# Performance work log

Measured on AMD Instinct MI355X. Metric: run time of the kernel, lower is better.

## Reference

```python
import jax, jax.numpy as jnp
import numpy as np

T_STEPS, BATCH, DX, DH = 128, 128, 1024, 1024
N_GATES = 5


def setup_inputs() -> dict:
    key = jax.random.key(0)
    ks = jax.random.split(key, 4)
    scale_x = 1.0 / np.sqrt(DX)
    scale_h = 1.0 / np.sqrt(DH)
    inputs = jax.random.normal(ks[0], (T_STEPS, BATCH, DX), dtype=jnp.float32)
    memories = jax.random.normal(ks[1], (T_STEPS, BATCH, DH), dtype=jnp.float32)
    h0 = jnp.zeros((BATCH, DH), dtype=jnp.float32)
    c0 = jnp.zeros((BATCH, DH), dtype=jnp.float32)
    Wx = jax.random.normal(ks[2], (N_GATES * DH, DX), dtype=jnp.float32) * scale_x
    bx = jnp.zeros((N_GATES * DH,), dtype=jnp.float32)
    Wh = jax.random.normal(ks[3], (N_GATES * DH, DH), dtype=jnp.float32) * scale_h
    # forget-gate bias (second chunk) initialized to 1, as in reset_parameters_
    bh = jnp.zeros((N_GATES * DH,), dtype=jnp.float32).at[DH:2 * DH].set(1.0)
    return {"inputs": inputs, "memories": memories, "h0": h0, "c0": c0,
            "Wx": Wx, "bx": bx, "Wh": Wh, "bh": bh}


def reference(inputs, memories, h0, c0, Wx, bx, Wh, bh):
    # EpLSTMCell.loop: time-major scan of the custom gated cell.
    # Gate order: I, F, G, O, R (tied forget gate: it = 1 - ft).
    def step(carry, inp):
        h, c = carry
        xt, mt = inp
        gx = jnp.dot(xt, Wx.T) + bx      # [B, 5*Dh]
        gh = jnp.dot(h, Wh.T) + bh       # [B, 5*Dh]
        Xi, Xf, Xg, Xo, Xr = jnp.split(gx, N_GATES, axis=-1)
        Hi, Hf, Hg, Ho, Hr = jnp.split(gh, N_GATES, axis=-1)
        ft = jax.nn.sigmoid(Xf + Hf)
        ot = jax.nn.sigmoid(Xo + Ho)
        it = 1.0 - ft                    # tied forget gate
        gt = jnp.tanh(Xg + Hg)
        rt = jax.nn.sigmoid(Xr + Hr)     # episodic memory gate
        ct = ft * c + it * gt + rt * jnp.tanh(mt)
        ht = ot * jnp.tanh(ct)
        return (ht, ct), ht

    (_, _), outs = jax.lax.scan(step, (h0, c0), (inputs, memories))
    return outs  # [T, B, Dh]
```

## Files before the change

### kernel.cpp

```cpp
#include <hip/hip_runtime.h>

#define T_STEPS 128
#define BATCH   128
#define DX      1024
#define DH      1024
#define BDH     (BATCH * DH)
#define BDX     (BATCH * DX)
#define PLW     40

typedef __attribute__((ext_vector_type(8)))  short short8;
typedef __attribute__((ext_vector_type(16))) float f32x16;
typedef __attribute__((ext_vector_type(4)))  float f32x4v;
typedef __attribute__((ext_vector_type(2)))  float f32x2;
typedef __attribute__((ext_vector_type(4)))  unsigned u32x4;

static __device__ __forceinline__ unsigned short f2bf(float f) {
    union { float f; unsigned u; } v; v.f = f;
    unsigned r = v.u + 0x7fffu + ((v.u >> 16) & 1u);
    return (unsigned short)(r >> 16);
}
static __device__ __forceinline__ short8 pack_bf16x8(f32x4v lo, f32x4v hi) {
    union { unsigned short u[8]; short8 v; } pk;
    pk.u[0]=f2bf(lo[0]); pk.u[1]=f2bf(lo[1]); pk.u[2]=f2bf(lo[2]); pk.u[3]=f2bf(lo[3]);
    pk.u[4]=f2bf(hi[0]); pk.u[5]=f2bf(hi[1]); pk.u[6]=f2bf(hi[2]); pk.u[7]=f2bf(hi[3]);
    return pk.v;
}
static __device__ __forceinline__ float sigf(float x) {
    float u = __expf(-fabsf(x));
    float b = 1.0f / (1.0f + u);
    return x >= 0.0f ? b : 1.0f - b;
}
static __device__ __forceinline__ float tanhfast(float x) {
    float u = __expf(-2.0f * fabsf(x));
    float r = (1.0f - u) / (1.0f + u);
    return x >= 0.0f ? r : -r;
}


__global__ __launch_bounds__(256) void prep_x(const float* __restrict__ x,
                                              unsigned short* __restrict__ Xb) {
    const size_t i8 = ((size_t)blockIdx.x * 256 + threadIdx.x) * 8;
    f32x4v lo = __builtin_nontemporal_load((const f32x4v*)(x + i8));
    f32x4v hi = __builtin_nontemporal_load((const f32x4v*)(x + i8 + 4));
    short8 v = pack_bf16x8(lo, hi);
    __builtin_nontemporal_store(v, (short8*)(Xb + i8));
}

__global__ __launch_bounds__(256) void init_seed(const float* __restrict__ h0,
                                                 unsigned short* __restrict__ hseq,
                                                 unsigned* __restrict__ gflag) {
    const int i = blockIdx.x * 256 + threadIdx.x;
    if (i < BDH) hseq[i] = f2bf(h0[i]);
    if (blockIdx.x < 2) gflag[blockIdx.x * 256 + threadIdx.x] = 0;
}

__global__ __launch_bounds__(128) void prep_wxp(const float* __restrict__ Wx,
                                                const float* __restrict__ bx,
                                                const float* __restrict__ bh,
                                                unsigned short* __restrict__ Wxp,
                                                float* __restrict__ bp) {
    const int p = blockIdx.x;
    const int js = p >> 5, g = (p >> 3) & 3, jj = p & 7;
    const int srow = (g + 1) * 1024 + js * 8 + jj;
    const int k = threadIdx.x * 8;
    f32x4v lo = __builtin_nontemporal_load((const f32x4v*)(Wx + (size_t)srow * DX + k));
    f32x4v hi = __builtin_nontemporal_load((const f32x4v*)(Wx + (size_t)srow * DX + k + 4));
    short8 v = pack_bf16x8(lo, hi);
    __builtin_nontemporal_store(v, (short8*)(Wxp + (size_t)p * 1024 + k));
    if (threadIdx.x == 0) bp[p] = bx[srow] + bh[srow];
}

template<bool XBF16>
__global__ __launch_bounds__(256, 1) void gx_prepass2(
    const void* __restrict__ xsrc, const unsigned short* __restrict__ Wxp,
    const float* __restrict__ bp, _Float16* __restrict__ Gx)
{
    extern __shared__ char sm[];
    _Float16* pl16 = (_Float16*)(sm + 131072);

    const int bid = blockIdx.x;
    const int c  = bid & 7;
    const int jp = bid >> 3;
    const int tid = threadIdx.x;

    {
        const int row = tid >> 2;
        const int chunk = tid & 3;
        const int sw = (row & 7) << 4;
        const unsigned short* src = Wxp + (size_t)(jp * 64 + row) * 1024;
        char* dst = sm + row * 2048;
        #pragma unroll
        for (int j = 0; j < 32; ++j) {
            const int off = chunk * 16 + j * 64;
            short8 v = __builtin_nontemporal_load((const short8*)(src + (off >> 1)));
            *(short8*)(dst + (off ^ sw)) = v;
        }
    }

    const int rrow = tid >> 1;
    const int jjb  = (tid & 1) * 4;
    float bias_f[2][16];
    #pragma unroll
    for (int jsl = 0; jsl < 2; ++jsl)
        #pragma unroll
        for (int q = 0; q < 4; ++q)
            #pragma unroll
            for (int g = 0; g < 4; ++g)
                bias_f[jsl][q * 4 + g] = bp[(jp * 2 + jsl) * 32 + g * 8 + (jjb + q)];

    const int wave = tid >> 6, lane = tid & 63;
    const int k8 = (lane >> 5) * 8;
    const char* wrow0 = sm + (lane & 31) * 2048;
    const char* wrow1 = wrow0 + 32 * 2048;
    const int sw2 = ((lane & 31) & 7) << 4;
    __syncthreads();

    for (int i = 0; i < 16; ++i) {
        const int mt = c * 16 + i;
        const int arow = mt * 128 + wave * 32 + (lane & 31);
        f32x16 a00 = {}, a01 = {}, a10 = {}, a11 = {};

        if (XBF16) {
            const unsigned short* xp = (const unsigned short*)xsrc + (size_t)arow * 1024 + k8;
            #pragma unroll 8
            for (int ks = 0; ks < 64; ++ks) {
                short8 a  = *(const short8*)(xp + ks * 16);
                short8 b0 = *(const short8*)(wrow0 + ((ks * 32 + k8 * 2) ^ sw2));
                short8 b1 = *(const short8*)(wrow1 + ((ks * 32 + k8 * 2) ^ sw2));
                if (ks & 1) {
                    a01 = __builtin_amdgcn_mfma_f32_32x32x16_bf16(a, b0, a01, 0, 0, 0);
                    a11 = __builtin_amdgcn_mfma_f32_32x32x16_bf16(a, b1, a11, 0, 0, 0);
                } else {
                    a00 = __builtin_amdgcn_mfma_f32_32x32x16_bf16(a, b0, a00, 0, 0, 0);
                    a10 = __builtin_amdgcn_mfma_f32_32x32x16_bf16(a, b1, a10, 0, 0, 0);
                }
            }
        } else {
            const float* Af = (const float*)xsrc + (size_t)arow * 1024 + k8;
            #pragma unroll 8
            for (int ks = 0; ks < 64; ++ks) {
                f32x4v lo = *(const f32x4v*)(Af + ks * 16);
                f32x4v hi = *(const f32x4v*)(Af + ks * 16 + 4);
                union { unsigned u32[4]; short8 v; } pk;
                pk.u32[0] = __builtin_amdgcn_perm(__float_as_uint(lo[1]), __float_as_uint(lo[0]), 0x07060302u);
                pk.u32[1] = __builtin_amdgcn_perm(__float_as_uint(lo[3]), __float_as_uint(lo[2]), 0x07060302u);
                pk.u32[2] = __builtin_amdgcn_perm(__float_as_uint(hi[1]), __float_as_uint(hi[0]), 0x07060302u);
                pk.u32[3] = __builtin_amdgcn_perm(__float_as_uint(hi[3]), __float_as_uint(hi[2]), 0x07060302u);
                short8 b0 = *(const short8*)(wrow0 + ((ks * 32 + k8 * 2) ^ sw2));
                short8 b1 = *(const short8*)(wrow1 + ((ks * 32 + k8 * 2) ^ sw2));
                if (ks & 1) {
                    a01 = __builtin_amdgcn_mfma_f32_32x32x16_bf16(pk.v, b0, a01, 0, 0, 0);
                    a11 = __builtin_amdgcn_mfma_f32_32x32x16_bf16(pk.v, b1, a11, 0, 0, 0);
                } else {
                    a00 = __builtin_amdgcn_mfma_f32_32x32x16_bf16(pk.v, b0, a00, 0, 0, 0);
                    a10 = __builtin_amdgcn_mfma_f32_32x32x16_bf16(pk.v, b1, a10, 0, 0, 0);
                }
            }
        }
        f32x16 r0 = a00 + a01;
        f32x16 r1 = a10 + a11;

        #pragma unroll
        for (int ii = 0; ii < 16; ++ii) {
            const int rowc = (ii & 3) + 8 * (ii >> 2) + 4 * (lane >> 5);
            pl16[(wave * 32 + rowc) * 72 + (lane & 31)]      = (_Float16)r0[ii];
            pl16[(wave * 32 + rowc) * 72 + 32 + (lane & 31)] = (_Float16)r1[ii];
        }
        __syncthreads();

        #pragma unroll
        for (int jsl = 0; jsl < 2; ++jsl) {
            union { _Float16 h[16]; u32x4 q[2]; } V;
            #pragma unroll
            for (int q = 0; q < 4; ++q)
                #pragma unroll
                for (int g = 0; g < 4; ++g)
                    V.h[q * 4 + g] = (_Float16)(
                        (float)pl16[rrow * 72 + jsl * 32 + g * 8 + (jjb + q)]
                        + bias_f[jsl][q * 4 + g]);
            _Float16* dst = Gx + ((size_t)(mt * 128 + rrow) * 4096
                                  + (jp * 2 + jsl) * 32 + jjb * 4);
            __builtin_nontemporal_store(V.q[0], (u32x4*)dst);
            __builtin_nontemporal_store(V.q[1], (u32x4*)(dst + 8));
        }
        __syncthreads();
    }
}

__global__ __launch_bounds__(256, 1) void eplstm_h(
    const _Float16* __restrict__ Gx,  const float* __restrict__ mem,
    const float* __restrict__ Wh,     const float* __restrict__ c0,
    unsigned short* __restrict__ hseq, float* __restrict__ out,
    unsigned* __restrict__ gflag)
{
    extern __shared__ char smem[];
    float* pl = (float*)(smem + 65536);

    const int bid = blockIdx.x;
    const int js = bid >> 1, bhh = bid & 1;
    const int tid = threadIdx.x;

    {
        const int row = tid >> 3;
        const int g = row >> 3, jj = row & 7;
        const int srow = (g + 1) * 1024 + js * 8 + jj;
        const int sw = (row & 7) << 4;
        const float* W = Wh + (size_t)srow * 1024;
        char* dst = smem + row * 2048;
        #pragma unroll
        for (int it = 0; it < 16; ++it) {
            const int k = (tid & 7) * 128 + it * 8;
            f32x4v lo = __builtin_nontemporal_load((const f32x4v*)(W + k));
            f32x4v hi = __builtin_nontemporal_load((const f32x4v*)(W + k + 4));
            short8 v = pack_bf16x8(lo, hi);
            *(short8*)(dst + ((k * 2) ^ sw)) = v;
        }
    }

    const int e0 = tid * 2;
    const int row_e = e0 >> 3;
    const int jj0 = e0 & 7;
    const int brow = bhh * 64 + row_e;
    const size_t obase = (size_t)brow * DH + js * 8 + jj0;
    const int mh_e = row_e >> 5, r_e = row_e & 31;
    float2 creg = *(const float2*)(c0 + obase);

    const int wave = tid >> 6, lane = tid & 63;
    const int mh = wave >> 1, kh = wave & 1;
    const int arow = bhh * 64 + mh * 32 + (lane & 31);
    const int k8 = (lane >> 5) * 8;
    const char* wrow = smem + (lane & 31) * 2048;
    const int sw2 = ((lane & 31) & 7) << 4;
    const int kbyte0 = (kh * 512 + k8) * 2;
    const int p = lane & 31;
    const int word = (p & 7) * 4 + (p >> 3);
    float* plw = pl + wave * 32 * PLW;
    unsigned long long* fb = (unsigned long long*)(gflag + bhh * 128);

    __syncthreads();

    for (int t = 0; t < T_STEPS; ++t) {
        u32x4 gxv = __builtin_nontemporal_load(
            (const u32x4*)(Gx + ((size_t)(t * BATCH + brow) * 4096 + js * 32 + jj0 * 4)));
        f32x2 mv = __builtin_nontemporal_load(
            (const f32x2*)(mem + (size_t)t * BDH + obase));

        if (t > 0) {
            if (wave == 0) {
                for (;;) {
                    unsigned long long fv = __hip_atomic_load(
                        &fb[lane], __ATOMIC_RELAXED, __HIP_MEMORY_SCOPE_AGENT);
                    if (__all(((unsigned)fv >= (unsigned)t) &&
                              ((unsigned)(fv >> 32) >= (unsigned)t))) break;
                    __builtin_amdgcn_s_sleep(4);
                }
            }
            __syncthreads();
        }

        const unsigned short* hp = hseq + (size_t)t * BDH + (size_t)arow * DH + kh * 512 + k8;
        f32x16 a0 = {}, a1 = {};
        #pragma unroll 16
        for (int ks = 0; ks < 32; ++ks) {
            short8 a = *(const short8*)(hp + ks * 16);
            short8 b = *(const short8*)(wrow + ((kbyte0 + ks * 32) ^ sw2));
            if (ks & 1) a1 = __builtin_amdgcn_mfma_f32_32x32x16_bf16(a, b, a1, 0, 0, 0);
            else        a0 = __builtin_amdgcn_mfma_f32_32x32x16_bf16(a, b, a0, 0, 0, 0);
        }
        f32x16 r = a0 + a1;
        #pragma unroll
        for (int ii = 0; ii < 16; ++ii) {
            const int rowc = (ii & 3) + 8 * (ii >> 2) + 4 * (lane >> 5);
            plw[rowc * PLW + word] = r[ii];
        }
        __syncthreads();

        float4 p0A = *(const float4*)(pl + (((mh_e << 1) | 0) * 32 + r_e) * PLW + (jj0 + 0) * 4);
        float4 p0B = *(const float4*)(pl + (((mh_e << 1) | 1) * 32 + r_e) * PLW + (jj0 + 0) * 4);
        float4 p1A = *(const float4*)(pl + (((mh_e << 1) | 0) * 32 + r_e) * PLW + (jj0 + 1) * 4);
        float4 p1B = *(const float4*)(pl + (((mh_e << 1) | 1) * 32 + r_e) * PLW + (jj0 + 1) * 4);
        union { u32x4 u; _Float16 h[8]; } G; G.u = gxv;

        float hv[2];
        {
            const float gF = (float)G.h[0] + p0A.x + p0B.x;
            const float gG = (float)G.h[1] + p0A.y + p0B.y;
            const float gO = (float)G.h[2] + p0A.z + p0B.z;
            const float gR = (float)G.h[3] + p0A.w + p0B.w;
            const float ft = sigf(gF), ot = sigf(gO), rt = sigf(gR);
            const float gt = tanhfast(gG);
            const float cv = ft * creg.x + (1.f - ft) * gt + rt * tanhfast(mv[0]);
            creg.x = cv;
            hv[0] = ot * tanhfast(cv);
        }
        {
            const float gF = (float)G.h[4] + p1A.x + p1B.x;
            const float gG = (float)G.h[5] + p1A.y + p1B.y;
            const float gO = (float)G.h[6] + p1A.z + p1B.z;
            const float gR = (float)G.h[7] + p1A.w + p1B.w;
            const float ft = sigf(gF), ot = sigf(gO), rt = sigf(gR);
            const float gt = tanhfast(gG);
            const float cv = ft * creg.y + (1.f - ft) * gt + rt * tanhfast(mv[1]);
            creg.y = cv;
            hv[1] = ot * tanhfast(cv);
        }
        const unsigned hp2 = (unsigned)f2bf(hv[0]) | ((unsigned)f2bf(hv[1]) << 16);
        __hip_atomic_store((unsigned*)(hseq + (size_t)(t + 1) * BDH + obase), hp2,
                           __ATOMIC_RELAXED, __HIP_MEMORY_SCOPE_AGENT);
        f32x2 hvv = { hv[0], hv[1] };
        __builtin_nontemporal_store(hvv, (f32x2*)(out + (size_t)t * BDH + obase));

        asm volatile("s_waitcnt vmcnt(0)" ::: "memory");
        __syncthreads();
        if (tid == 0 && t < T_STEPS - 1) {
            __hip_atomic_store(&gflag[bhh * 128 + js], (unsigned)(t + 1),
                               __ATOMIC_RELAXED, __HIP_MEMORY_SCOPE_AGENT);
        }
    }
}

template<bool XBF16>
__global__ __launch_bounds__(256, 1) void eplstm_persistent(
    const void*  __restrict__ xsrc, const float* __restrict__ mem,
    const float* __restrict__ Wx,   const float* __restrict__ Wh,
    const float* __restrict__ bxp,  const float* __restrict__ bhp,
    const float* __restrict__ c0,
    unsigned short* __restrict__ hseq, float* __restrict__ out,
    unsigned* __restrict__ bar)
{
    extern __shared__ char smem[];
    float* pl = reinterpret_cast<float*>(smem + 131072);

    const int bid = blockIdx.x;
    const int js  = bid >> 1;
    const int bhh = bid & 1;
    const int tid = threadIdx.x;

    {
        const int prow = tid >> 3;
        const int g = prow >> 3, jj = prow & 7;
        const int srow = (g + 1) * 1024 + js * 8 + jj;
        const int kc = (tid & 7) * 256;
        const int sw = (prow & 7) << 4;
        for (int it = 0; it < 32; ++it) {
            const int k = kc + it * 8;
            const float* src = (k < DX) ? (Wx + (size_t)srow * DX + k)
                                        : (Wh + (size_t)srow * DH + (k - DX));
            f32x4v lo = *(const f32x4v*)(src);
            f32x4v hi = *(const f32x4v*)(src + 4);
            short8 v = pack_bf16x8(lo, hi);
            *reinterpret_cast<short8*>(smem + prow * 4096 + ((k * 2) ^ sw)) = v;
        }
    }

    const int e0   = tid * 2;
    const int bl   = e0 >> 3;
    const int jj0  = e0 & 7;
    const int brow_g = bhh * 64 + bl;
    const size_t oidx = (size_t)brow_g * DH + js * 8 + jj0;
    float biasv[2][4];
    #pragma unroll
    for (int e2 = 0; e2 < 2; ++e2)
        #pragma unroll
        for (int g = 0; g < 4; ++g) {
            const int srow = (g + 1) * 1024 + js * 8 + jj0 + e2;
            biasv[e2][g] = bxp[srow] + bhp[srow];
        }
    float2 creg = *reinterpret_cast<const float2*>(c0 + oidx);
    const int mh_e = bl >> 5, rr = bl & 31;

    const int wave = tid >> 6;
    const int lane = tid & 63;
    const int mh = wave >> 1, kh = wave & 1;
    const int arow   = bhh * 64 + mh * 32 + (lane & 31);
    const int k8     = (lane >> 5) * 8;
    const int brow   = lane & 31;
    const char* bbase = smem + brow * 4096;
    const int swz    = (brow & 7) << 4;
    const int kbyte0 = kh * 2048 + k8 * 2;

    __syncthreads();

    for (int t = 0; t < T_STEPS; ++t) {
        f32x16 ac0 = {}, ac1 = {}, ac2 = {}, ac3 = {};
        if (XBF16 || kh == 1) {
            const unsigned short* Ab = kh
                ? (hseq + (size_t)t * BDH + (size_t)arow * DH + k8)
                : ((const unsigned short*)xsrc + (size_t)t * BDX + (size_t)arow * DX + k8);
            #pragma unroll 8
            for (int ks = 0; ks < 64; ++ks) {
                short8 a = *reinterpret_cast<const short8*>(Ab + ks * 16);
                short8 b = *reinterpret_cast<const short8*>(bbase + ((kbyte0 + ks * 32) ^ swz));
                if      ((ks & 3) == 0) ac0 = __builtin_amdgcn_mfma_f32_32x32x16_bf16(a, b, ac0, 0, 0, 0);
                else if ((ks & 3) == 1) ac1 = __builtin_amdgcn_mfma_f32_32x32x16_bf16(a, b, ac1, 0, 0, 0);
                else if ((ks & 3) == 2) ac2 = __builtin_amdgcn_mfma_f32_32x32x16_bf16(a, b, ac2, 0, 0, 0);
                else                    ac3 = __builtin_amdgcn_mfma_f32_32x32x16_bf16(a, b, ac3, 0, 0, 0);
            }
        } else {
            const float* Af = (const float*)xsrc + (size_t)t * BDX + (size_t)arow * DX + k8;
            #pragma unroll 4
            for (int ks = 0; ks < 64; ++ks) {
                f32x4v lo = *(const f32x4v*)(Af + ks * 16);
                f32x4v hi = *(const f32x4v*)(Af + ks * 16 + 4);
                short8 a = pack_bf16x8(lo, hi);
                short8 b = *reinterpret_cast<const short8*>(bbase + ((kbyte0 + ks * 32) ^ swz));
                if      ((ks & 3) == 0) ac0 = __builtin_amdgcn_mfma_f32_32x32x16_bf16(a, b, ac0, 0, 0, 0);
                else if ((ks & 3) == 1) ac1 = __builtin_amdgcn_mfma_f32_32x32x16_bf16(a, b, ac1, 0, 0, 0);
                else if ((ks & 3) == 2) ac2 = __builtin_amdgcn_mfma_f32_32x32x16_bf16(a, b, ac2, 0, 0, 0);
                else                    ac3 = __builtin_amdgcn_mfma_f32_32x32x16_bf16(a, b, ac3, 0, 0, 0);
            }
        }
        f32x16 r = (ac0 + ac1) + (ac2 + ac3);

        #pragma unroll
        for (int i = 0; i < 16; ++i) {
            const int row = (i & 3) + 8 * (i >> 2) + 4 * (lane >> 5);
            pl[(wave * 32 + row) * 33 + brow] = r[i];
        }
        __syncthreads();

        const float2 mt2 = *reinterpret_cast<const float2*>(mem + (size_t)t * BDH + oidx);
        float hv[2];
        #pragma unroll
        for (int e2 = 0; e2 < 2; ++e2) {
            const int jj = jj0 + e2;
            float gs[4];
            #pragma unroll
            for (int g = 0; g < 4; ++g) {
                const int col = g * 8 + jj;
                gs[g] = pl[((mh_e * 2 + 0) * 32 + rr) * 33 + col]
                      + pl[((mh_e * 2 + 1) * 32 + rr) * 33 + col]
                      + biasv[e2][g];
            }
            const float ft = 1.f / (1.f + expf(-gs[0]));
            const float gt = tanhf(gs[1]);
            const float ot = 1.f / (1.f + expf(-gs[2]));
            const float rt = 1.f / (1.f + expf(-gs[3]));
            const float cin = e2 ? creg.y : creg.x;
            const float mv  = e2 ? mt2.y : mt2.x;
            const float cv = ft * cin + (1.f - ft) * gt + rt * tanhf(mv);
            if (e2) creg.y = cv; else creg.x = cv;
            hv[e2] = ot * tanhf(cv);
        }
        *reinterpret_cast<float2*>(out + (size_t)t * BDH + oidx) = make_float2(hv[0], hv[1]);
        const unsigned hp = (unsigned)f2bf(hv[0]) | ((unsigned)f2bf(hv[1]) << 16);
        __hip_atomic_store((unsigned*)(hseq + (size_t)(t + 1) * BDH + oidx), hp,
                           __ATOMIC_RELAXED, __HIP_MEMORY_SCOPE_AGENT);

        __syncthreads();
        if (t < T_STEPS - 1) {
            if (tid == 0) {
                const unsigned want = (unsigned)(t + 1);
                const unsigned arrived = __hip_atomic_fetch_add(
                    &bar[bhh * 32], 1u, __ATOMIC_RELAXED, __HIP_MEMORY_SCOPE_AGENT);
                if (arrived == want * 128u - 1u) {
                    __hip_atomic_store(&bar[64 + bhh * 32], want,
                                       __ATOMIC_RELAXED, __HIP_MEMORY_SCOPE_AGENT);
                } else {
                    while (__hip_atomic_load(&bar[64 + bhh * 32],
                                             __ATOMIC_RELAXED, __HIP_MEMORY_SCOPE_AGENT) < want)
                        __builtin_amdgcn_s_sleep(2);
                }
            }
            __syncthreads();
        }
    }
}

extern "C" void kernel_launch(void* const* d_in, const int* in_sizes, int n_in,
                              void* d_out, int out_size, void* d_ws, size_t ws_size,
                              hipStream_t stream) {
    const float* inputs   = (const float*)d_in[0];
    const float* memories = (const float*)d_in[1];
    const float* h0       = (const float*)d_in[2];
    const float* c0       = (const float*)d_in[3];
    const float* Wx       = (const float*)d_in[4];
    const float* bx       = (const float*)d_in[5];
    const float* Wh       = (const float*)d_in[6];
    const float* bh_      = (const float*)d_in[7];
    float* outp = (float*)d_out;

    char* ws = (char*)d_ws;
    size_t off = 0;
    auto alloc = [&](size_t bytes) {
        char* p = ws + off;
        off = (off + bytes + 255) & ~(size_t)255;
        return p;
    };
    unsigned*       gflag = (unsigned*)alloc(512 * sizeof(unsigned));
    unsigned short* hseq  = (unsigned short*)alloc((size_t)(T_STEPS + 1) * BDH * 2);

    const size_t wxp_b  = (size_t)4096 * 1024 * 2;
    const size_t bp_b   = 4096 * 4;
    const size_t gx_b   = (size_t)16384 * 4096 * 2;
    const size_t xb_b   = (size_t)T_STEPS * BDX * 2;
    const size_t need_base = off + wxp_b + 256 + bp_b + 256 + gx_b + 256;
    const size_t need_xb   = need_base + xb_b + 256;

    if (ws_size >= need_base) {
        unsigned short* Wxp = (unsigned short*)alloc(wxp_b);
        float*          bp  = (float*)alloc(bp_b);
        _Float16*       Gx  = (_Float16*)alloc(gx_b);
        const bool use_xb = (ws_size >= need_xb);
        unsigned short* Xb = use_xb ? (unsigned short*)alloc(xb_b) : nullptr;

        init_seed<<<512, 256, 0, stream>>>(h0, hseq, gflag);
        prep_wxp<<<4096, 128, 0, stream>>>(Wx, bx, bh_, Wxp, bp);

        const unsigned pre_smem = 131072 + 128 * 72 * 2;
        if (use_xb) {
            prep_x<<<8192, 256, 0, stream>>>(inputs, Xb);
            (void)hipFuncSetAttribute((const void*)gx_prepass2<true>,
                                      hipFuncAttributeMaxDynamicSharedMemorySize, pre_smem);
            gx_prepass2<true><<<512, 256, pre_smem, stream>>>((const void*)Xb, Wxp, bp, Gx);
        } else {
            (void)hipFuncSetAttribute((const void*)gx_prepass2<false>,
                                      hipFuncAttributeMaxDynamicSharedMemorySize, pre_smem);
            gx_prepass2<false><<<512, 256, pre_smem, stream>>>((const void*)inputs, Wxp, bp, Gx);
        }

        const unsigned smem_bytes = 65536 + 4 * 32 * PLW * 4;
        (void)hipFuncSetAttribute((const void*)eplstm_h,
                                  hipFuncAttributeMaxDynamicSharedMemorySize, smem_bytes);
        void* kargs[] = { (void*)&Gx, (void*)&memories, (void*)&Wh, (void*)&c0,
                          (void*)&hseq, (void*)&outp, (void*)&gflag };
        hipError_t err = hipLaunchCooperativeKernel((const void*)eplstm_h, dim3(256),
                                                    dim3(256), kargs, smem_bytes, stream);
        if (err != hipSuccess) {
            eplstm_h<<<256, 256, smem_bytes, stream>>>(Gx, memories, Wh, c0,
                                                       hseq, outp, gflag);
        }
    } else {
        const bool use_xb = (ws_size >= off + xb_b + 256);
        unsigned short* Xb = use_xb ? (unsigned short*)alloc(xb_b) : nullptr;

        init_seed<<<512, 256, 0, stream>>>(h0, hseq, gflag);
        if (use_xb) prep_x<<<8192, 256, 0, stream>>>(inputs, Xb);

        const unsigned smem_bytes = 131072 + 9216 + 9216 + 64;
        const void* xsrc = use_xb ? (const void*)Xb : (const void*)inputs;
        if (use_xb) {
            (void)hipFuncSetAttribute((const void*)eplstm_persistent<true>,
                                      hipFuncAttributeMaxDynamicSharedMemorySize, smem_bytes);
            void* kargs[] = { (void*)&xsrc, (void*)&memories, (void*)&Wx, (void*)&Wh,
                              (void*)&bx, (void*)&bh_, (void*)&c0, (void*)&hseq,
                              (void*)&outp, (void*)&gflag };
            hipError_t err = hipLaunchCooperativeKernel(
                (const void*)eplstm_persistent<true>, dim3(256), dim3(256),
                kargs, smem_bytes, stream);
            if (err != hipSuccess) {
                eplstm_persistent<true><<<256, 256, smem_bytes, stream>>>(
                    xsrc, memories, Wx, Wh, bx, bh_, c0, hseq, outp, gflag);
            }
        } else {
            (void)hipFuncSetAttribute((const void*)eplstm_persistent<false>,
                                      hipFuncAttributeMaxDynamicSharedMemorySize, smem_bytes);
            void* kargs[] = { (void*)&xsrc, (void*)&memories, (void*)&Wx, (void*)&Wh,
                              (void*)&bx, (void*)&bh_, (void*)&c0, (void*)&hseq,
                              (void*)&outp, (void*)&gflag };
            hipError_t err = hipLaunchCooperativeKernel(
                (const void*)eplstm_persistent<false>, dim3(256), dim3(256),
                kargs, smem_bytes, stream);
            if (err != hipSuccess) {
                eplstm_persistent<false><<<256, 256, smem_bytes, stream>>>(
                    xsrc, memories, Wx, Wh, bx, bh_, c0, hseq, outp, gflag);
            }
        }
    }
}
```

Baseline: 1.563 ms.

## Register-resident Wh, precomputed tanh(mem), smaller Gx prepass tiles, reordered flag store

The recurrent kernel now holds its Wh slice in registers (32 short8 per lane) instead of shared memory, and remaps block-to-(js, batch-half) indices. A new prep kernel precomputes tanh(memories) in fp16 so the serial loop reads half the bytes and skips a tanh per element. The Gx prepass moves to 32-column tiles with two blocks per CU and 1024 blocks. The output store now comes after the flag release, and the spin sleep is shorter, to cut time on the per-step critical path. These add register pressure, an extra pass over the memories tensor, and fp16 rounding of tanh(mem).

```diff
diff --git a/kernel.cpp b/kernel.cpp
--- a/kernel.cpp
+++ b/kernel.cpp
@@ -13,6 +13,7 @@
 typedef __attribute__((ext_vector_type(4)))  float f32x4v;
 typedef __attribute__((ext_vector_type(2)))  float f32x2;
 typedef __attribute__((ext_vector_type(4)))  unsigned u32x4;
+typedef __attribute__((ext_vector_type(2)))  _Float16 f16x2;
 
 static __device__ __forceinline__ unsigned short f2bf(float f) {
     union { float f; unsigned u; } v; v.f = f;
@@ -44,6 +45,19 @@
     f32x4v hi = __builtin_nontemporal_load((const f32x4v*)(x + i8 + 4));
     short8 v = pack_bf16x8(lo, hi);
     __builtin_nontemporal_store(v, (short8*)(Xb + i8));
+}
+
+__global__ __launch_bounds__(256) void prep_tm(const float* __restrict__ mem,
+                                               _Float16* __restrict__ TM) {
+    const size_t i8 = ((size_t)blockIdx.x * 256 + threadIdx.x) * 8;
+    f32x4v lo = __builtin_nontemporal_load((const f32x4v*)(mem + i8));
+    f32x4v hi = __builtin_nontemporal_load((const f32x4v*)(mem + i8 + 4));
+    union { _Float16 h[8]; u32x4 q; } V;
+    #pragma unroll
+    for (int j = 0; j < 4; ++j) V.h[j]     = (_Float16)tanhfast(lo[j]);
+    #pragma unroll
+    for (int j = 0; j < 4; ++j) V.h[4 + j] = (_Float16)tanhfast(hi[j]);
+    __builtin_nontemporal_store(V.q, (u32x4*)(TM + i8));
 }
 
 __global__ __launch_bounds__(256) void init_seed(const float* __restrict__ h0,
@@ -71,69 +85,59 @@
 }
 
 template<bool XBF16>
-__global__ __launch_bounds__(256, 1) void gx_prepass2(
+__global__ __launch_bounds__(256, 2) void gx_prepass3(
     const void* __restrict__ xsrc, const unsigned short* __restrict__ Wxp,
     const float* __restrict__ bp, _Float16* __restrict__ Gx)
 {
     extern __shared__ char sm[];
-    _Float16* pl16 = (_Float16*)(sm + 131072);
+    _Float16* pl16 = (_Float16*)(sm + 65536);
 
     const int bid = blockIdx.x;
     const int c  = bid & 7;
-    const int jp = bid >> 3;
+    const int js = bid >> 3;
     const int tid = threadIdx.x;
 
     {
-        const int row = tid >> 2;
-        const int chunk = tid & 3;
+        const int row = tid >> 3;
+        const int koff = (tid & 7) * 128;
         const int sw = (row & 7) << 4;
-        const unsigned short* src = Wxp + (size_t)(jp * 64 + row) * 1024;
+        const unsigned short* src = Wxp + (size_t)(js * 32 + row) * 1024 + koff;
         char* dst = sm + row * 2048;
         #pragma unroll
-        for (int j = 0; j < 32; ++j) {
-            const int off = chunk * 16 + j * 64;
-            short8 v = __builtin_nontemporal_load((const short8*)(src + (off >> 1)));
-            *(short8*)(dst + (off ^ sw)) = v;
+        for (int it = 0; it < 16; ++it) {
+            short8 v = __builtin_nontemporal_load((const short8*)(src + it * 8));
+            *(short8*)(dst + (((koff + it * 8) * 2) ^ sw)) = v;
         }
     }
 
     const int rrow = tid >> 1;
     const int jjb  = (tid & 1) * 4;
-    float bias_f[2][16];
+    float bias_f[16];
     #pragma unroll
-    for (int jsl = 0; jsl < 2; ++jsl)
-        #pragma unroll
-        for (int q = 0; q < 4; ++q)
-            #pragma unroll
-            for (int g = 0; g < 4; ++g)
-                bias_f[jsl][q * 4 + g] = bp[(jp * 2 + jsl) * 32 + g * 8 + (jjb + q)];
+    for (int q = 0; q < 4; ++q)
+        #pragma unroll
+        for (int g = 0; g < 4; ++g)
+            bias_f[q * 4 + g] = bp[js * 32 + g * 8 + (jjb + q)];
 
     const int wave = tid >> 6, lane = tid & 63;
     const int k8 = (lane >> 5) * 8;
-    const char* wrow0 = sm + (lane & 31) * 2048;
-    const char* wrow1 = wrow0 + 32 * 2048;
+    const char* wrow = sm + (lane & 31) * 2048;
     const int sw2 = ((lane & 31) & 7) << 4;
     __syncthreads();
 
     for (int i = 0; i < 16; ++i) {
         const int mt = c * 16 + i;
         const int arow = mt * 128 + wave * 32 + (lane & 31);
-        f32x16 a00 = {}, a01 = {}, a10 = {}, a11 = {};
+        f32x16 a0 = {}, a1 = {};
 
         if (XBF16) {
             const unsigned short* xp = (const unsigned short*)xsrc + (size_t)arow * 1024 + k8;
             #pragma unroll 8
             for (int ks = 0; ks < 64; ++ks) {
-                short8 a  = *(const short8*)(xp + ks * 16);
-                short8 b0 = *(const short8*)(wrow0 + ((ks * 32 + k8 * 2) ^ sw2));
-                short8 b1 = *(const short8*)(wrow1 + ((ks * 32 + k8 * 2) ^ sw2));
-                if (ks & 1) {
-                    a01 = __builtin_amdgcn_mfma_f32_32x32x16_bf16(a, b0, a01, 0, 0, 0);
-                    a11 = __builtin_amdgcn_mfma_f32_32x32x16_bf16(a, b1, a11, 0, 0, 0);
-                } else {
-                    a00 = __builtin_amdgcn_mfma_f32_32x32x16_bf16(a, b0, a00, 0, 0, 0);
-                    a10 = __builtin_amdgcn_mfma_f32_32x32x16_bf16(a, b1, a10, 0, 0, 0);
-                }
+                short8 a = *(const short8*)(xp + ks * 16);
+                short8 b = *(const short8*)(wrow + ((ks * 32 + k8 * 2) ^ sw2));
+                if (ks & 1) a1 = __builtin_amdgcn_mfma_f32_32x32x16_bf16(a, b, a1, 0, 0, 0);
+                else        a0 = __builtin_amdgcn_mfma_f32_32x32x16_bf16(a, b, a0, 0, 0, 0);
             }
         } else {
             const float* Af = (const float*)xsrc + (size_t)arow * 1024 + k8;
@@ -146,40 +150,29 @@
                 pk.u32[1] = __builtin_amdgcn_perm(__float_as_uint(lo[3]), __float_as_uint(lo[2]), 0x07060302u);
                 pk.u32[2] = __builtin_amdgcn_perm(__float_as_uint(hi[1]), __float_as_uint(hi[0]), 0x07060302u);
                 pk.u32[3] = __builtin_amdgcn_perm(__float_as_uint(hi[3]), __float_as_uint(hi[2]), 0x07060302u);
-                short8 b0 = *(const short8*)(wrow0 + ((ks * 32 + k8 * 2) ^ sw2));
-                short8 b1 = *(const short8*)(wrow1 + ((ks * 32 + k8 * 2) ^ sw2));
-                if (ks & 1) {
-                    a01 = __builtin_amdgcn_mfma_f32_32x32x16_bf16(pk.v, b0, a01, 0, 0, 0);
-                    a11 = __builtin_amdgcn_mfma_f32_32x32x16_bf16(pk.v, b1, a11, 0, 0, 0);
-                } else {
-                    a00 = __builtin_amdgcn_mfma_f32_32x32x16_bf16(pk.v, b0, a00, 0, 0, 0);
-                    a10 = __builtin_amdgcn_mfma_f32_32x32x16_bf16(pk.v, b1, a10, 0, 0, 0);
-                }
-            }
-        }
-        f32x16 r0 = a00 + a01;
-        f32x16 r1 = a10 + a11;
+                short8 b = *(const short8*)(wrow + ((ks * 32 + k8 * 2) ^ sw2));
+                if (ks & 1) a1 = __builtin_amdgcn_mfma_f32_32x32x16_bf16(pk.v, b, a1, 0, 0, 0);
+                else        a0 = __builtin_amdgcn_mfma_f32_32x32x16_bf16(pk.v, b, a0, 0, 0, 0);
+            }
+        }
+        f32x16 r = a0 + a1;
 
         #pragma unroll
         for (int ii = 0; ii < 16; ++ii) {
             const int rowc = (ii & 3) + 8 * (ii >> 2) + 4 * (lane >> 5);
-            pl16[(wave * 32 + rowc) * 72 + (lane & 31)]      = (_Float16)r0[ii];
-            pl16[(wave * 32 + rowc) * 72 + 32 + (lane & 31)] = (_Float16)r1[ii];
+            pl16[(wave * 32 + rowc) * 40 + (lane & 31)] = (_Float16)r[ii];
         }
         __syncthreads();
 
-        #pragma unroll
-        for (int jsl = 0; jsl < 2; ++jsl) {
+        {
             union { _Float16 h[16]; u32x4 q[2]; } V;
             #pragma unroll
             for (int q = 0; q < 4; ++q)
                 #pragma unroll
                 for (int g = 0; g < 4; ++g)
                     V.h[q * 4 + g] = (_Float16)(
-                        (float)pl16[rrow * 72 + jsl * 32 + g * 8 + (jjb + q)]
-                        + bias_f[jsl][q * 4 + g]);
-            _Float16* dst = Gx + ((size_t)(mt * 128 + rrow) * 4096
-                                  + (jp * 2 + jsl) * 32 + jjb * 4);
+                        (float)pl16[rrow * 40 + g * 8 + (jjb + q)] + bias_f[q * 4 + g]);
+            _Float16* dst = Gx + ((size_t)(mt * 128 + rrow) * 4096 + js * 32 + jjb * 4);
             __builtin_nontemporal_store(V.q[0], (u32x4*)dst);
             __builtin_nontemporal_store(V.q[1], (u32x4*)(dst + 8));
         }
@@ -187,33 +180,40 @@
     }
 }
 
+template<bool USE_TM>
 __global__ __launch_bounds__(256, 1) void eplstm_h(
-    const _Float16* __restrict__ Gx,  const float* __restrict__ mem,
+    const _Float16* __restrict__ Gx,  const void* __restrict__ tmv,
     const float* __restrict__ Wh,     const float* __restrict__ c0,
     unsigned short* __restrict__ hseq, float* __restrict__ out,
     unsigned* __restrict__ gflag)
 {
-    extern __shared__ char smem[];
-    float* pl = (float*)(smem + 65536);
+    __shared__ float pl[4 * 32 * PLW];
 
     const int bid = blockIdx.x;
-    const int js = bid >> 1, bhh = bid & 1;
+    const int js  = (bid >> 3) * 4 + (bid & 3);
+    const int bhh = (bid >> 2) & 1;
     const int tid = threadIdx.x;
 
+    const int wave = tid >> 6, lane = tid & 63;
+    const int mh = wave >> 1, kh = wave & 1;
+    const int arow = bhh * 64 + mh * 32 + (lane & 31);
+    const int k8 = (lane >> 5) * 8;
+    const int p = lane & 31;
+    const int word = (p & 7) * 4 + (p >> 3);
+    float* plw = pl + wave * 32 * PLW;
+    unsigned long long* fb = (unsigned long long*)(gflag + bhh * 128);
+
+    short8 breg[32];
     {
-        const int row = tid >> 3;
-        const int g = row >> 3, jj = row & 7;
-        const int srow = (g + 1) * 1024 + js * 8 + jj;
-        const int sw = (row & 7) << 4;
-        const float* W = Wh + (size_t)srow * 1024;
-        char* dst = smem + row * 2048;
-        #pragma unroll
-        for (int it = 0; it < 16; ++it) {
-            const int k = (tid & 7) * 128 + it * 8;
-            f32x4v lo = __builtin_nontemporal_load((const f32x4v*)(W + k));
-            f32x4v hi = __builtin_nontemporal_load((const f32x4v*)(W + k + 4));
-            short8 v = pack_bf16x8(lo, hi);
-            *(short8*)(dst + ((k * 2) ^ sw)) = v;
+        const int r = lane & 31;
+        const int g = r >> 3, jj = r & 7;
+        const float* Wrow = Wh + (size_t)((g + 1) * 1024 + js * 8 + jj) * 1024
+                          + kh * 512 + k8;
+        #pragma unroll
+        for (int ks = 0; ks < 32; ++ks) {
+            f32x4v lo = *(const f32x4v*)(Wrow + ks * 16);
+            f32x4v hi = *(const f32x4v*)(Wrow + ks * 16 + 4);
+            breg[ks] = pack_bf16x8(lo, hi);
         }
     }
 
@@ -225,25 +225,18 @@
     const int mh_e = row_e >> 5, r_e = row_e & 31;
     float2 creg = *(const float2*)(c0 + obase);
 
-    const int wave = tid >> 6, lane = tid & 63;
-    const int mh = wave >> 1, kh = wave & 1;
-    const int arow = bhh * 64 + mh * 32 + (lane & 31);
-    const int k8 = (lane >> 5) * 8;
-    const char* wrow = smem + (lane & 31) * 2048;
-    const int sw2 = ((lane & 31) & 7) << 4;
-    const int kbyte0 = (kh * 512 + k8) * 2;
-    const int p = lane & 31;
-    const int word = (p & 7) * 4 + (p >> 3);
-    float* plw = pl + wave * 32 * PLW;
-    unsigned long long* fb = (unsigned long long*)(gflag + bhh * 128);
-
-    __syncthreads();
-
     for (int t = 0; t < T_STEPS; ++t) {
         u32x4 gxv = __builtin_nontemporal_load(
             (const u32x4*)(Gx + ((size_t)(t * BATCH + brow) * 4096 + js * 32 + jj0 * 4)));
-        f32x2 mv = __builtin_nontemporal_load(
-            (const f32x2*)(mem + (size_t)t * BDH + obase));
+        f16x2 tm2 = {};
+        f32x2 mv = {};
+        if (USE_TM) {
+            tm2 = __builtin_nontemporal_load(
+                (const f16x2*)((const _Float16*)tmv + (size_t)t * BDH + obase));
+        } else {
+            mv = __builtin_nontemporal_load(
+                (const f32x2*)((const float*)tmv + (size_t)t * BDH + obase));
+        }
 
         if (t > 0) {
             if (wave == 0) {
@@ -252,7 +245,7 @@
                         &fb[lane], __ATOMIC_RELAXED, __HIP_MEMORY_SCOPE_AGENT);
                     if (__all(((unsigned)fv >= (unsigned)t) &&
                               ((unsigned)(fv >> 32) >= (unsigned)t))) break;
-                    __builtin_amdgcn_s_sleep(4);
+                    __builtin_amdgcn_s_sleep(2);
                 }
             }
             __syncthreads();
@@ -260,12 +253,11 @@
 
         const unsigned short* hp = hseq + (size_t)t * BDH + (size_t)arow * DH + kh * 512 + k8;
         f32x16 a0 = {}, a1 = {};
-        #pragma unroll 16
+        #pragma unroll
         for (int ks = 0; ks < 32; ++ks) {
             short8 a = *(const short8*)(hp + ks * 16);
-            short8 b = *(const short8*)(wrow + ((kbyte0 + ks * 32) ^ sw2));
-            if (ks & 1) a1 = __builtin_amdgcn_mfma_f32_32x32x16_bf16(a, b, a1, 0, 0, 0);
-            else        a0 = __builtin_amdgcn_mfma_f32_32x32x16_bf16(a, b, a0, 0, 0, 0);
+            if (ks & 1) a1 = __builtin_amdgcn_mfma_f32_32x32x16_bf16(a, breg[ks], a1, 0, 0, 0);
+            else        a0 = __builtin_amdgcn_mfma_f32_32x32x16_bf16(a, breg[ks], a0, 0, 0, 0);
         }
         f32x16 r = a0 + a1;
         #pragma unroll
@@ -275,10 +267,10 @@
         }
         __syncthreads();
 
-        float4 p0A = *(const float4*)(pl + (((mh_e << 1) | 0) * 32 + r_e) * PLW + (jj0 + 0) * 4);
-        float4 p0B = *(const float4*)(pl + (((mh_e << 1) | 1) * 32 + r_e) * PLW + (jj0 + 0) * 4);
-        float4 p1A = *(const float4*)(pl + (((mh_e << 1) | 0) * 32 + r_e) * PLW + (jj0 + 1) * 4);
-        float4 p1B = *(const float4*)(pl + (((mh_e << 1) | 1) * 32 + r_e) * PLW + (jj0 + 1) * 4);
+        float4 p0A = *(const float4*)(pl + ((((mh_e << 1) | 0) * 32 + r_e) * PLW + (jj0 + 0) * 4));
+        float4 p0B = *(const float4*)(pl + ((((mh_e << 1) | 1) * 32 + r_e) * PLW + (jj0 + 0) * 4));
+        float4 p1A = *(const float4*)(pl + ((((mh_e << 1) | 0) * 32 + r_e) * PLW + (jj0 + 1) * 4));
+        float4 p1B = *(const float4*)(pl + ((((mh_e << 1) | 1) * 32 + r_e) * PLW + (jj0 + 1) * 4));
         union { u32x4 u; _Float16 h[8]; } G; G.u = gxv;
 
         float hv[2];
@@ -289,7 +281,8 @@
             const float gR = (float)G.h[3] + p0A.w + p0B.w;
             const float ft = sigf(gF), ot = sigf(gO), rt = sigf(gR);
             const float gt = tanhfast(gG);
-            const float cv = ft * creg.x + (1.f - ft) * gt + rt * tanhfast(mv[0]);
+            const float tmv0 = USE_TM ? (float)tm2[0] : tanhfast(mv[0]);
+            const float cv = ft * creg.x + (1.f - ft) * gt + rt * tmv0;
             creg.x = cv;
             hv[0] = ot * tanhfast(cv);
         }
@@ -300,22 +293,22 @@
             const float gR = (float)G.h[7] + p1A.w + p1B.w;
             const float ft = sigf(gF), ot = sigf(gO), rt = sigf(gR);
             const float gt = tanhfast(gG);
-            const float cv = ft * creg.y + (1.f - ft) * gt + rt * tanhfast(mv[1]);
+            const float tmv1 = USE_TM ? (float)tm2[1] : tanhfast(mv[1]);
+            const float cv = ft * creg.y + (1.f - ft) * gt + rt * tmv1;
             creg.y = cv;
             hv[1] = ot * tanhfast(cv);
         }
         const unsigned hp2 = (unsigned)f2bf(hv[0]) | ((unsigned)f2bf(hv[1]) << 16);
         __hip_atomic_store((unsigned*)(hseq + (size_t)(t + 1) * BDH + obase), hp2,
                            __ATOMIC_RELAXED, __HIP_MEMORY_SCOPE_AGENT);
-        f32x2 hvv = { hv[0], hv[1] };
-        __builtin_nontemporal_store(hvv, (f32x2*)(out + (size_t)t * BDH + obase));
-
         asm volatile("s_waitcnt vmcnt(0)" ::: "memory");
         __syncthreads();
         if (tid == 0 && t < T_STEPS - 1) {
             __hip_atomic_store(&gflag[bhh * 128 + js], (unsigned)(t + 1),
                                __ATOMIC_RELAXED, __HIP_MEMORY_SCOPE_AGENT);
         }
+        f32x2 hvv = { hv[0], hv[1] };
+        __builtin_nontemporal_store(hvv, (f32x2*)(out + (size_t)t * BDH + obase));
     }
 }
 
@@ -437,14 +430,14 @@
             const float ot = 1.f / (1.f + expf(-gs[2]));
             const float rt = 1.f / (1.f + expf(-gs[3]));
             const float cin = e2 ? creg.y : creg.x;
-            const float mv  = e2 ? mt2.y : mt2.x;
-            const float cv = ft * cin + (1.f - ft) * gt + rt * tanhf(mv);
+            const float mvv = e2 ? mt2.y : mt2.x;
+            const float cv = ft * cin + (1.f - ft) * gt + rt * tanhf(mvv);
             if (e2) creg.y = cv; else creg.x = cv;
             hv[e2] = ot * tanhf(cv);
         }
         *reinterpret_cast<float2*>(out + (size_t)t * BDH + oidx) = make_float2(hv[0], hv[1]);
-        const unsigned hp = (unsigned)f2bf(hv[0]) | ((unsigned)f2bf(hv[1]) << 16);
-        __hip_atomic_store((unsigned*)(hseq + (size_t)(t + 1) * BDH + oidx), hp,
+        const unsigned hpk = (unsigned)f2bf(hv[0]) | ((unsigned)f2bf(hv[1]) << 16);
+        __hip_atomic_store((unsigned*)(hseq + (size_t)(t + 1) * BDH + oidx), hpk,
                            __ATOMIC_RELAXED, __HIP_MEMORY_SCOPE_AGENT);
 
         __syncthreads();
@@ -494,8 +487,10 @@
     const size_t bp_b   = 4096 * 4;
     const size_t gx_b   = (size_t)16384 * 4096 * 2;
     const size_t xb_b   = (size_t)T_STEPS * BDX * 2;
+    const size_t tm_b   = (size_t)T_STEPS * BDH * 2;
     const size_t need_base = off + wxp_b + 256 + bp_b + 256 + gx_b + 256;
     const size_t need_xb   = need_base + xb_b + 256;
+    const size_t need_tm   = need_xb + tm_b + 256;
 
     if (ws_size >= need_base) {
         unsigned short* Wxp = (unsigned short*)alloc(wxp_b);
@@ -503,32 +498,40 @@
         _Float16*       Gx  = (_Float16*)alloc(gx_b);
         const bool use_xb = (ws_size >= need_xb);
         unsigned short* Xb = use_xb ? (unsigned short*)alloc(xb_b) : nullptr;
+        const bool use_tm = (ws_size >= need_tm);
+        _Float16* TM = use_tm ? (_Float16*)alloc(tm_b) : nullptr;
 
         init_seed<<<512, 256, 0, stream>>>(h0, hseq, gflag);
         prep_wxp<<<4096, 128, 0, stream>>>(Wx, bx, bh_, Wxp, bp);
-
-        const unsigned pre_smem = 131072 + 128 * 72 * 2;
+        if (use_tm) prep_tm<<<8192, 256, 0, stream>>>(memories, TM);
+
+        const unsigned pre_smem = 65536 + 128 * 40 * 2;
         if (use_xb) {
             prep_x<<<8192, 256, 0, stream>>>(inputs, Xb);
-            (void)hipFuncSetAttribute((const void*)gx_prepass2<true>,
+            (void)hipFuncSetAttribute((const void*)gx_prepass3<true>,
                                       hipFuncAttributeMaxDynamicSharedMemorySize, pre_smem);
-            gx_prepass2<true><<<512, 256, pre_smem, stream>>>((const void*)Xb, Wxp, bp, Gx);
+            gx_prepass3<true><<<1024, 256, pre_smem, stream>>>((const void*)Xb, Wxp, bp, Gx);
         } else {
-            (void)hipFuncSetAttribute((const void*)gx_prepass2<false>,
+            (void)hipFuncSetAttribute((const void*)gx_prepass3<false>,
                                       hipFuncAttributeMaxDynamicSharedMemorySize, pre_smem);
-            gx_prepass2<false><<<512, 256, pre_smem, stream>>>((const void*)inputs, Wxp, bp, Gx);
-        }
-
-        const unsigned smem_bytes = 65536 + 4 * 32 * PLW * 4;
-        (void)hipFuncSetAttribute((const void*)eplstm_h,
-                                  hipFuncAttributeMaxDynamicSharedMemorySize, smem_bytes);
-        void* kargs[] = { (void*)&Gx, (void*)&memories, (void*)&Wh, (void*)&c0,
-                          (void*)&hseq, (void*)&outp, (void*)&gflag };
-        hipError_t err = hipLaunchCooperativeKernel((const void*)eplstm_h, dim3(256),
-                                                    dim3(256), kargs, smem_bytes, stream);
-        if (err != hipSuccess) {
-            eplstm_h<<<256, 256, smem_bytes, stream>>>(Gx, memories, Wh, c0,
-                                                       hseq, outp, gflag);
+            gx_prepass3<false><<<1024, 256, pre_smem, stream>>>((const void*)inputs, Wxp, bp, Gx);
+        }
+
+        const void* tmv = use_tm ? (const void*)TM : (const void*)memories;
+        if (use_tm) {
+            void* kargs[] = { (void*)&Gx, (void*)&tmv, (void*)&Wh, (void*)&c0,
+                              (void*)&hseq, (void*)&outp, (void*)&gflag };
+            hipError_t err = hipLaunchCooperativeKernel((const void*)eplstm_h<true>,
+                                                        dim3(256), dim3(256), kargs, 0, stream);
+            if (err != hipSuccess)
+                eplstm_h<true><<<256, 256, 0, stream>>>(Gx, tmv, Wh, c0, hseq, outp, gflag);
+        } else {
+            void* kargs[] = { (void*)&Gx, (void*)&tmv, (void*)&Wh, (void*)&c0,
+                              (void*)&hseq, (void*)&outp, (void*)&gflag };
+            hipError_t err = hipLaunchCooperativeKernel((const void*)eplstm_h<false>,
+                                                        dim3(256), dim3(256), kargs, 0, stream);
+            if (err != hipSuccess)
+                eplstm_h<false><<<256, 256, 0, stream>>>(Gx, tmv, Wh, c0, hseq, outp, gflag);
         }
     } else {
         const bool use_xb = (ws_size >= off + xb_b + 256);
```

Result: slower. 1.625 ms (+4.0%).
